# Performance work log

Measured on AMD Instinct MI355X. Metric: run time of the kernel, lower is better.

The kernel has to match this reference:

```python
import jax, jax.numpy as jnp
import numpy as np
from jax import lax

DIM = 96
HEADS = 4
HID = int(DIM * 2.66)  # 255
EPS_LN = 1e-5
EPS_NORM = 1e-12


def _ln(x, w, b):
    # channel-wise LayerNorm over c of (b,c,h,w) (equivalent to to_3d -> LN(c) -> to_4d)
    mu = x.mean(axis=1, keepdims=True)
    var = ((x - mu) ** 2).mean(axis=1, keepdims=True)
    return (x - mu) / jnp.sqrt(var + EPS_LN) * w[None, :, None, None] + b[None, :, None, None]


def _c1x1(w, x):
    # 1x1 conv, no bias: w (out,in), x (b,in,h,w)
    return jnp.einsum('oc,bchw->bohw', w, x)


def _l2norm(x):
    # F.normalize along last dim (pixels), eps=1e-12
    n = jnp.sqrt(jnp.sum(x * x, axis=-1, keepdims=True))
    return x / jnp.maximum(n, EPS_NORM)


def setup_inputs() -> dict:
    key = jax.random.key(0)
    ks = jax.random.split(key, 10)
    B, H, W = 4, 256, 256
    s = 0.02
    return {
        'x': jax.random.normal(ks[0], (B, DIM, H, W), jnp.float32),
        'svp_fea': jax.random.normal(ks[1], (B, 3, H, W), jnp.float32),
        'norm1_w': jnp.ones((DIM,), jnp.float32),
        'norm1_b': jnp.zeros((DIM,), jnp.float32),
        'qkv_w': jax.random.normal(ks[2], (3 * DIM, DIM), jnp.float32) * s,
        'qkv_dw_w': jax.random.normal(ks[3], (3 * DIM, 1, 3, 3), jnp.float32) * s,
        'svp_w': jax.random.normal(ks[4], (3 * HEADS, 3), jnp.float32) * s,
        'temperature': jnp.ones((HEADS, 1, 1), jnp.float32),
        'proj_out_w': jax.random.normal(ks[5], (DIM, DIM + 3 * HEADS), jnp.float32) * s,
        'norm2_w': jnp.ones((DIM,), jnp.float32),
        'norm2_b': jnp.zeros((DIM,), jnp.float32),
        'ffn1_w': jax.random.normal(ks[6], (HID, DIM), jnp.float32) * s,
        'ffn2_w': jax.random.normal(ks[7], (HID, DIM), jnp.float32) * s,
        'ffn_out_w': jax.random.normal(ks[8], (DIM, HID), jnp.float32) * s,
    }


def reference(x, svp_fea, norm1_w, norm1_b, qkv_w, qkv_dw_w, svp_w, temperature,
              proj_out_w, norm2_w, norm2_b, ffn1_w, ffn2_w, ffn_out_w):
    b, c, h, w = x.shape
    hw = h * w
    # --- IlluminationGuideAttention ---
    xn = _ln(x, norm1_w, norm1_b)
    qkv = _c1x1(qkv_w, xn)
    qkv = lax.conv_general_dilated(
        qkv, qkv_dw_w, window_strides=(1, 1), padding='SAME',
        feature_group_count=3 * DIM, dimension_numbers=('NCHW', 'OIHW', 'NCHW'))
    q, k, v = jnp.split(qkv, 3, axis=1)
    svp_q = _c1x1(svp_w, svp_fea)

    def heads(t):
        return t.reshape(b, HEADS, -1, hw)  # b head c (h w)

    q = _l2norm(heads(q))          # (b,H,ch,hw)
    k = _l2norm(heads(k))
    svp_q = _l2norm(heads(svp_q))  # (b,H,3,hw)
    v = heads(v)
    q = jnp.concatenate([q, svp_q], axis=2)  # (b,H,ch+3,hw)

    attn = jnp.einsum('bhcn,bhdn->bhcd', q, k) * temperature[None]
    attn = jax.nn.softmax(attn, axis=-1)
    out = jnp.einsum('bhcd,bhdn->bhcn', attn, v).reshape(b, -1, h, w)
    x = x + _c1x1(proj_out_w, out)

    # --- DualGatedFeedForward ---
    xn = _ln(x, norm2_w, norm2_b)
    p1 = _c1x1(ffn1_w, xn)
    p2 = _c1x1(ffn2_w, xn)
    g = p1 * jax.nn.sigmoid(p2) + p2 * jax.nn.gelu(p1, approximate=False)
    return x + _c1x1(ffn_out_w, g)
```

## Files before the change

kernel.cpp:

```cpp
#include <hip/hip_runtime.h>


namespace {
constexpr int kB = 4;
constexpr int kC = 96;
constexpr int kHW = 65536;
constexpr int kNP = kB * kHW;
constexpr int kQKVC = 288;
constexpr int kNH = 4;
constexpr int kCH = 24;
constexpr int kQC = 27;
constexpr int kHID = 255;
constexpr int kSTR = 40;
constexpr int kQKSPLIT = 32;
}

typedef __attribute__((ext_vector_type(8))) short short8;
typedef __attribute__((ext_vector_type(8))) unsigned short ushort8;
typedef __attribute__((ext_vector_type(4))) float floatx4;

__device__ __forceinline__ float bf2f(unsigned short u) {
  return __uint_as_float(((unsigned int)u) << 16);
}
__device__ __forceinline__ unsigned short f2bf(float f) {
  unsigned int i = __float_as_uint(f);
  i += 0x7fffu + ((i >> 16) & 1u);
  return (unsigned short)(i >> 16);
}

__global__ void k_zero(float* __restrict__ p, int n) {
  const int i = blockIdx.x * blockDim.x + threadIdx.x;
  if (i < n) p[i] = 0.f;
}
__global__ void k_fill0_f32(float* __restrict__ p, int n) {
  const int i = blockIdx.x * blockDim.x + threadIdx.x;
  if (i < n) p[i] = 0.f;
}

__global__ __launch_bounds__(256) void k_wconv(
    const float* __restrict__ qkvw, const float* __restrict__ projw,
    const float* __restrict__ w1, const float* __restrict__ w2,
    const float* __restrict__ fw, unsigned short* __restrict__ qb,
    unsigned short* __restrict__ pb, unsigned short* __restrict__ w1b,
    unsigned short* __restrict__ w2b, unsigned short* __restrict__ fwb) {
  int i = blockIdx.x * 256 + threadIdx.x;
  if (i < 27648) { qb[i] = f2bf(qkvw[i]); return; }
  i -= 27648;
  if (i < 12288) {
    const int r = i >> 7, k = i & 127;
    pb[i] = (k < 108) ? f2bf(projw[r * 108 + k]) : (unsigned short)0;
    return;
  }
  i -= 12288;
  if (i < 24576) { w1b[i] = (i < 24480) ? f2bf(w1[i]) : (unsigned short)0; return; }
  i -= 24576;
  if (i < 24576) { w2b[i] = (i < 24480) ? f2bf(w2[i]) : (unsigned short)0; return; }
  i -= 24576;
  {
    const int r = i >> 8, k = i & 255;
    fwb[i] = (k < 255) ? f2bf(fw[r * 255 + k]) : (unsigned short)0;
  }
}

__global__ __launch_bounds__(256) void k_ln1_apply(
    const float* __restrict__ x, const float* __restrict__ nw,
    const float* __restrict__ nb, unsigned short* __restrict__ A) {
  const int pg = blockIdx.x * 256 + threadIdx.x;
  const int b = pg >> 16, p = pg & (kHW - 1);
  const float* xb = x + (size_t)b * kC * kHW + p;
  float v[kC];
  float s = 0.f, s2 = 0.f;
  #pragma unroll
  for (int c = 0; c < kC; ++c) {
    v[c] = xb[(size_t)c * kHW];
    s += v[c];
    s2 = fmaf(v[c], v[c], s2);
  }
  const float m = s * (1.f / kC);
  const float var = s2 * (1.f / kC) - m * m;
  const float rstd = rsqrtf(var + 1e-5f);
  unsigned short* ob = A + ((size_t)b * kQKVC + 192) * kHW + p;
  #pragma unroll
  for (int c = 0; c < kC; ++c) {
    ob[(size_t)c * kHW] = f2bf((v[c] - m) * rstd * nw[c] + nb[c]);
  }
}

__global__ __launch_bounds__(256) void k_ln2_stats(
    const unsigned short* __restrict__ x2, float* __restrict__ mu, float* __restrict__ rs) {
  const int pg = blockIdx.x * 256 + threadIdx.x;
  const int b = pg >> 16, p = pg & (kHW - 1);
  const unsigned short* xb = x2 + (size_t)b * kC * kHW + p;
  float s = 0.f, s2 = 0.f;
  for (int c = 0; c < kC; ++c) { const float v = bf2f(xb[(size_t)c * kHW]); s += v; s2 += v * v; }
  const float m = s * (1.f / kC);
  const float var = s2 * (1.f / kC) - m * m;
  mu[pg] = m;
  rs[pg] = rsqrtf(var + 1e-5f);
}

__global__ __launch_bounds__(256) void k_gemm_qkv(
    const unsigned short* __restrict__ xn1base, const unsigned short* __restrict__ qb,
    int grp, unsigned short* __restrict__ bufC) {
  __shared__ __align__(16) unsigned short As[96 * kSTR];
  __shared__ __align__(16) unsigned short Bs[128 * kSTR];
  const int tid = threadIdx.x;
  const int b = blockIdx.y;
  const int p0 = blockIdx.x * 128;
  const int wave = tid >> 6, lane = tid & 63, ln16 = lane & 15, quad = lane >> 4;
  floatx4 acc[6][2];
  #pragma unroll
  for (int i = 0; i < 6; ++i) { acc[i][0] = (floatx4)(0.f); acc[i][1] = (floatx4)(0.f); }
  const int rB = tid >> 3, c0 = (tid & 7) * 16;
  const int pos = rB ^ ((tid & 3) << 3);
  const int q0 = (quad ^ ((wave * 2) & 3)) << 3;
  const int q1 = (quad ^ ((wave * 2 + 1) & 3)) << 3;
  for (int ks = 0; ks < 3; ++ks) {
    const int k0 = ks * 32;
    for (int idx = tid; idx < 384; idx += 256) {
      const int m = idx >> 2, ch = idx & 3;
      *(short8*)&As[m * kSTR + ch * 8] =
          *(const short8*)(qb + (size_t)(grp * 96 + m) * 96 + k0 + ch * 8);
    }
    {
      const unsigned short* src =
          xn1base + ((size_t)b * kQKVC + 192 + k0 + rB) * kHW + p0 + c0;
      const ushort8 u0 = ((const ushort8*)src)[0];
      const ushort8 u1 = ((const ushort8*)src)[1];
      #pragma unroll
      for (int e = 0; e < 8; ++e) {
        Bs[(c0 + e) * kSTR + pos] = u0[e];
        Bs[(c0 + 8 + e) * kSTR + pos] = u1[e];
      }
    }
    __syncthreads();
    short8 bfr0 = *(const short8*)&Bs[(wave * 32 + ln16) * kSTR + q0];
    short8 bfr1 = *(const short8*)&Bs[(wave * 32 + 16 + ln16) * kSTR + q1];
    #pragma unroll
    for (int ms = 0; ms < 6; ++ms) {
      const short8 afr = *(const short8*)&As[(ms * 16 + ln16) * kSTR + quad * 8];
      acc[ms][0] = __builtin_amdgcn_mfma_f32_16x16x32_bf16(afr, bfr0, acc[ms][0], 0, 0, 0);
      acc[ms][1] = __builtin_amdgcn_mfma_f32_16x16x32_bf16(afr, bfr1, acc[ms][1], 0, 0, 0);
    }
    __syncthreads();
  }
  unsigned short* ob = bufC + (size_t)b * kC * kHW;
  #pragma unroll
  for (int ms = 0; ms < 6; ++ms)
    #pragma unroll
    for (int ns = 0; ns < 2; ++ns)
      #pragma unroll
      for (int r = 0; r < 4; ++r) {
        const int R = ms * 16 + quad * 4 + r;
        const int P = p0 + wave * 32 + ns * 16 + ln16;
        ob[(size_t)R * kHW + P] = f2bf(acc[ms][ns][r]);
      }
}

__global__ __launch_bounds__(256) void k_gemm_proj(
    const unsigned short* __restrict__ qkv_post, const unsigned short* __restrict__ pb,
    const float* __restrict__ x, unsigned short* __restrict__ x2) {
  __shared__ __align__(16) unsigned short As[96 * kSTR];
  __shared__ __align__(16) unsigned short Bs[128 * kSTR];
  const int tid = threadIdx.x;
  const int b = blockIdx.y;
  const int p0 = blockIdx.x * 128;
  const int wave = tid >> 6, lane = tid & 63, ln16 = lane & 15, quad = lane >> 4;
  floatx4 acc[6][2];
  #pragma unroll
  for (int i = 0; i < 6; ++i) { acc[i][0] = (floatx4)(0.f); acc[i][1] = (floatx4)(0.f); }
  const int rB = tid >> 3, c0 = (tid & 7) * 16;
  const int pos = rB ^ ((tid & 3) << 3);
  const int q0 = (quad ^ ((wave * 2) & 3)) << 3;
  const int q1 = (quad ^ ((wave * 2 + 1) & 3)) << 3;
  for (int ks = 0; ks < 4; ++ks) {
    const int k0 = ks * 32;
    for (int idx = tid; idx < 384; idx += 256) {
      const int m = idx >> 2, ch = idx & 3;
      *(short8*)&As[m * kSTR + ch * 8] =
          *(const short8*)(pb + (size_t)m * 128 + k0 + ch * 8);
    }
    {
      const int k = k0 + rB;
      if (k < 108) {
        const unsigned short* src = qkv_post + ((size_t)b * kQKVC + k) * kHW + p0 + c0;
        const ushort8 u0 = ((const ushort8*)src)[0];
        const ushort8 u1 = ((const ushort8*)src)[1];
        #pragma unroll
        for (int e = 0; e < 8; ++e) {
          Bs[(c0 + e) * kSTR + pos] = u0[e];
          Bs[(c0 + 8 + e) * kSTR + pos] = u1[e];
        }
      } else {
        #pragma unroll
        for (int e = 0; e < 16; ++e) Bs[(c0 + e) * kSTR + pos] = 0;
      }
    }
    __syncthreads();
    short8 bfr0 = *(const short8*)&Bs[(wave * 32 + ln16) * kSTR + q0];
    short8 bfr1 = *(const short8*)&Bs[(wave * 32 + 16 + ln16) * kSTR + q1];
    #pragma unroll
    for (int ms = 0; ms < 6; ++ms) {
      const short8 afr = *(const short8*)&As[(ms * 16 + ln16) * kSTR + quad * 8];
      acc[ms][0] = __builtin_amdgcn_mfma_f32_16x16x32_bf16(afr, bfr0, acc[ms][0], 0, 0, 0);
      acc[ms][1] = __builtin_amdgcn_mfma_f32_16x16x32_bf16(afr, bfr1, acc[ms][1], 0, 0, 0);
    }
    __syncthreads();
  }
  #pragma unroll
  for (int ms = 0; ms < 6; ++ms)
    #pragma unroll
    for (int ns = 0; ns < 2; ++ns)
      #pragma unroll
      for (int r = 0; r < 4; ++r) {
        const int R = ms * 16 + quad * 4 + r;
        const int P = p0 + wave * 32 + ns * 16 + ln16;
        const size_t idx = ((size_t)b * kC + R) * kHW + P;
        x2[idx] = f2bf(acc[ms][ns][r] + x[idx]);
      }
}

__global__ __launch_bounds__(256) void k_gemm_gate(
    const unsigned short* __restrict__ x2, const float* __restrict__ mu_buf,
    const float* __restrict__ rs_buf, const float* __restrict__ nw,
    const float* __restrict__ nb, const unsigned short* __restrict__ w1b,
    const unsigned short* __restrict__ w2b, unsigned short* __restrict__ g) {
  __shared__ __align__(16) unsigned short Bs[3 * 128 * kSTR];
  __shared__ __align__(16) unsigned short As[128 * kSTR];
  __shared__ float mus[128], rss[128];
  const int tid = threadIdx.x;
  const int b = blockIdx.y;
  const int p0 = blockIdx.x * 128;
  if (tid < 128) {
    mus[tid] = mu_buf[(b << 16) + p0 + tid];
    rss[tid] = rs_buf[(b << 16) + p0 + tid];
  }
  __syncthreads();
  const int wave = tid >> 6, lane = tid & 63, ln16 = lane & 15, quad = lane >> 4;
  const int rB = tid >> 3, c0 = (tid & 7) * 16;
  const int pos = rB ^ ((tid & 3) << 3);
  const int q0 = (quad ^ ((wave * 2) & 3)) << 3;
  const int q1 = (quad ^ ((wave * 2 + 1) & 3)) << 3;
  #pragma unroll
  for (int ks = 0; ks < 3; ++ks) {
    const int k = ks * 32 + rB;
    const float wk = nw[k], bk = nb[k];
    const unsigned short* src = x2 + ((size_t)b * kC + k) * kHW + p0 + c0;
    const ushort8 u0 = ((const ushort8*)src)[0];
    const ushort8 u1 = ((const ushort8*)src)[1];
    unsigned short* bp = &Bs[ks * 128 * kSTR];
    #pragma unroll
    for (int e = 0; e < 8; ++e) {
      const int n0 = c0 + e, n1 = c0 + 8 + e;
      bp[n0 * kSTR + pos] = f2bf((bf2f(u0[e]) - mus[n0]) * rss[n0] * wk + bk);
      bp[n1 * kSTR + pos] = f2bf((bf2f(u1[e]) - mus[n1]) * rss[n1] * wk + bk);
    }
  }
  for (int grp = 0; grp < 4; ++grp) {
    const int i0 = grp * 64;
    floatx4 acc[8][2];
    #pragma unroll
    for (int i = 0; i < 8; ++i) { acc[i][0] = (floatx4)(0.f); acc[i][1] = (floatx4)(0.f); }
    #pragma unroll
    for (int ks = 0; ks < 3; ++ks) {
      for (int idx = tid; idx < 512; idx += 256) {
        const int m = idx >> 2, ch = idx & 3;
        const int ii = i0 + (m & 63);
        const unsigned short* wsrc =
            ((m < 64) ? w1b : w2b) + (size_t)ii * 96 + ks * 32 + ch * 8;
        *(short8*)&As[m * kSTR + ch * 8] = *(const short8*)wsrc;
      }
      __syncthreads();
      const unsigned short* bp = &Bs[ks * 128 * kSTR];
      short8 bfr0 = *(const short8*)&bp[(wave * 32 + ln16) * kSTR + q0];
      short8 bfr1 = *(const short8*)&bp[(wave * 32 + 16 + ln16) * kSTR + q1];
      #pragma unroll
      for (int ms = 0; ms < 8; ++ms) {
        const short8 afr = *(const short8*)&As[(ms * 16 + ln16) * kSTR + quad * 8];
        acc[ms][0] = __builtin_amdgcn_mfma_f32_16x16x32_bf16(afr, bfr0, acc[ms][0], 0, 0, 0);
        acc[ms][1] = __builtin_amdgcn_mfma_f32_16x16x32_bf16(afr, bfr1, acc[ms][1], 0, 0, 0);
      }
      __syncthreads();
    }
    #pragma unroll
    for (int ms = 0; ms < 4; ++ms)
      #pragma unroll
      for (int ns = 0; ns < 2; ++ns)
        #pragma unroll
        for (int r = 0; r < 4; ++r) {
          const int ii = i0 + ms * 16 + quad * 4 + r;
          if (ii < kHID) {
            const int P = p0 + wave * 32 + ns * 16 + ln16;
            const float p1 = acc[ms][ns][r], p2 = acc[ms + 4][ns][r];
            const float sig = 1.f / (1.f + __expf(-p2));
            const float gel = 0.5f * p1 * (1.f + erff(p1 * 0.70710678118f));
            g[((size_t)b * kHID + ii) * kHW + P] = f2bf(p1 * sig + p2 * gel);
          }
        }
  }
}

__global__ __launch_bounds__(256) void k_gemm_fout(
    const unsigned short* __restrict__ g, const unsigned short* __restrict__ fwb,
    const unsigned short* __restrict__ x2, float* __restrict__ out) {
  __shared__ __align__(16) unsigned short As[96 * kSTR];
  __shared__ __align__(16) unsigned short Bs[128 * kSTR];
  const int tid = threadIdx.x;
  const int b = blockIdx.y;
  const int p0 = blockIdx.x * 128;
  const int wave = tid >> 6, lane = tid & 63, ln16 = lane & 15, quad = lane >> 4;
  floatx4 acc[6][2];
  #pragma unroll
  for (int i = 0; i < 6; ++i) { acc[i][0] = (floatx4)(0.f); acc[i][1] = (floatx4)(0.f); }
  const int rB = tid >> 3, c0 = (tid & 7) * 16;
  const int pos = rB ^ ((tid & 3) << 3);
  const int q0 = (quad ^ ((wave * 2) & 3)) << 3;
  const int q1 = (quad ^ ((wave * 2 + 1) & 3)) << 3;
  for (int ks = 0; ks < 8; ++ks) {
    const int k0 = ks * 32;
    for (int idx = tid; idx < 384; idx += 256) {
      const int m = idx >> 2, ch = idx & 3;
      *(short8*)&As[m * kSTR + ch * 8] =
          *(const short8*)(fwb + (size_t)m * 256 + k0 + ch * 8);
    }
    {
      const int k = k0 + rB;
      if (k < kHID) {
        const unsigned short* src = g + ((size_t)b * kHID + k) * kHW + p0 + c0;
        const ushort8 u0 = ((const ushort8*)src)[0];
        const ushort8 u1 = ((const ushort8*)src)[1];
        #pragma unroll
        for (int e = 0; e < 8; ++e) {
          Bs[(c0 + e) * kSTR + pos] = u0[e];
          Bs[(c0 + 8 + e) * kSTR + pos] = u1[e];
        }
      } else {
        #pragma unroll
        for (int e = 0; e < 16; ++e) Bs[(c0 + e) * kSTR + pos] = 0;
      }
    }
    __syncthreads();
    short8 bfr0 = *(const short8*)&Bs[(wave * 32 + ln16) * kSTR + q0];
    short8 bfr1 = *(const short8*)&Bs[(wave * 32 + 16 + ln16) * kSTR + q1];
    #pragma unroll
    for (int ms = 0; ms < 6; ++ms) {
      const short8 afr = *(const short8*)&As[(ms * 16 + ln16) * kSTR + quad * 8];
      acc[ms][0] = __builtin_amdgcn_mfma_f32_16x16x32_bf16(afr, bfr0, acc[ms][0], 0, 0, 0);
      acc[ms][1] = __builtin_amdgcn_mfma_f32_16x16x32_bf16(afr, bfr1, acc[ms][1], 0, 0, 0);
    }
    __syncthreads();
  }
  #pragma unroll
  for (int ms = 0; ms < 6; ++ms)
    #pragma unroll
    for (int ns = 0; ns < 2; ++ns)
      #pragma unroll
      for (int r = 0; r < 4; ++r) {
        const int R = ms * 16 + quad * 4 + r;
        const int P = p0 + wave * 32 + ns * 16 + ln16;
        const size_t idx = ((size_t)b * kC + R) * kHW + P;
        out[idx] = acc[ms][ns][r] + bf2f(x2[idx]);
      }
}

__global__ __launch_bounds__(256) void k_dw(
    const unsigned short* __restrict__ buf, const float* __restrict__ dww,
    unsigned short* __restrict__ qkv_post, int gbase) {
  const int blk = blockIdx.x;
  const int plane = blk >> 5;
  const int y0 = (blk & 31) * 8;
  const int b = plane / kC, chl = plane % kC;
  const int t = threadIdx.x;
  const int y = y0 + (t >> 5);
  const int x0 = (t & 31) * 8;
  const unsigned short* in = buf + (size_t)plane * kHW;
  float w[9];
  #pragma unroll
  for (int i = 0; i < 9; ++i) w[i] = dww[(size_t)(gbase + chl) * 9 + i];
  float acc[8];
  #pragma unroll
  for (int j = 0; j < 8; ++j) acc[j] = 0.f;
  #pragma unroll
  for (int dy = -1; dy <= 1; ++dy) {
    const int yy = y + dy;
    if (yy < 0 || yy > 255) continue;
    const unsigned short* rp = in + yy * 256;
    float f[10];
    const ushort8 v = *(const ushort8*)(rp + x0);
    #pragma unroll
    for (int e = 0; e < 8; ++e) f[e + 1] = bf2f(v[e]);
    f[0] = (x0 > 0) ? bf2f(rp[x0 - 1]) : 0.f;
    f[9] = (x0 < 248) ? bf2f(rp[x0 + 8]) : 0.f;
    const float w0 = w[(dy + 1) * 3], w1 = w[(dy + 1) * 3 + 1], w2 = w[(dy + 1) * 3 + 2];
    #pragma unroll
    for (int j = 0; j < 8; ++j)
      acc[j] = fmaf(w0, f[j], fmaf(w1, f[j + 1], fmaf(w2, f[j + 2], acc[j])));
  }
  unsigned short* op = qkv_post + ((size_t)b * kQKVC + gbase + chl) * kHW + y * 256 + x0;
  ushort8 o;
  #pragma unroll
  for (int j = 0; j < 8; ++j) o[j] = f2bf(acc[j]);
  *(ushort8*)op = o;
}

__global__ __launch_bounds__(256) void k_svpq(
    const float* __restrict__ svp, const float* __restrict__ svpw,
    unsigned short* __restrict__ svpq) {
  const int pg = blockIdx.x * 256 + threadIdx.x;
  const int b = pg >> 16, p = pg & (kHW - 1);
  const float s0 = svp[((size_t)b * 3 + 0) * kHW + p];
  const float s1 = svp[((size_t)b * 3 + 1) * kHW + p];
  const float s2 = svp[((size_t)b * 3 + 2) * kHW + p];
  #pragma unroll
  for (int j = 0; j < 12; ++j) {
    const float v = svpw[j * 3] * s0 + svpw[j * 3 + 1] * s1 + svpw[j * 3 + 2] * s2;
    svpq[((size_t)b * 12 + j) * kHW + p] = f2bf(v);
  }
}

__global__ __launch_bounds__(256) void k_qk(
    const unsigned short* __restrict__ qkv_post, const unsigned short* __restrict__ svpq,
    float* __restrict__ spart, float* __restrict__ ssbuf) {
  const int bh = blockIdx.y, b = bh >> 2, h = bh & 3;
  const int tid = threadIdx.x;
  const int wave = tid >> 6, lane = tid & 63;
  const int l15 = lane & 15, gq = lane >> 4;
  const int pstart = blockIdx.x * 2048 + wave * 512;
  constexpr int NCH = 16;

  const unsigned short* pA0 =
      qkv_post + ((size_t)b * kQKVC + h * kCH + l15) * kHW + gq * 8;
  const unsigned short* pB0 =
      qkv_post + ((size_t)b * kQKVC + 96 + h * kCH + l15) * kHW + gq * 8;
  const int rA1 = 16 + l15, rB1 = 16 + l15;
  const bool vA1 = (rA1 < kQC), vB1 = (rB1 < kCH);
  const unsigned short* pA1 =
      (rA1 < kCH) ? qkv_post + ((size_t)b * kQKVC + h * kCH + rA1) * kHW + gq * 8
      : (rA1 < kQC) ? svpq + ((size_t)(b * 12 + h * 3 + (rA1 - kCH))) * kHW + gq * 8
                    : pA0;
  const unsigned short* pB1 =
      vB1 ? qkv_post + ((size_t)b * kQKVC + 96 + h * kCH + rB1) * kHW + gq * 8 : pB0;

  floatx4 c00 = (floatx4)(0.f), c01 = (floatx4)(0.f);
  floatx4 c10 = (floatx4)(0.f), c11 = (floatx4)(0.f);
  float ssA0 = 0.f, ssA1 = 0.f, ssB0 = 0.f, ssB1 = 0.f;
  const short8 kZ = (short8)(short)0;

  short8 a0 = *(const short8*)(pA0 + pstart);
  short8 b0 = *(const short8*)(pB0 + pstart);
  short8 a1 = vA1 ? *(const short8*)(pA1 + pstart) : kZ;
  short8 b1 = vB1 ? *(const short8*)(pB1 + pstart) : kZ;
  for (int c = 0; c < NCH; ++c) {
    const short8 ta0 = a0, tb0 = b0, ta1 = a1, tb1 = b1;
    if (c + 1 < NCH) {
      const int pn = pstart + (c + 1) * 32;
      a0 = *(const short8*)(pA0 + pn);
      b0 = *(const short8*)(pB0 + pn);
      a1 = vA1 ? *(const short8*)(pA1 + pn) : kZ;
      b1 = vB1 ? *(const short8*)(pB1 + pn) : kZ;
    }
    c00 = __builtin_amdgcn_mfma_f32_16x16x32_bf16(ta0, tb0, c00, 0, 0, 0);
    c01 = __builtin_amdgcn_mfma_f32_16x16x32_bf16(ta0, tb1, c01, 0, 0, 0);
    c10 = __builtin_amdgcn_mfma_f32_16x16x32_bf16(ta1, tb0, c10, 0, 0, 0);
    c11 = __builtin_amdgcn_mfma_f32_16x16x32_bf16(ta1, tb1, c11, 0, 0, 0);
    #pragma unroll
    for (int e = 0; e < 8; ++e) {
      const float v0 = bf2f((unsigned short)ta0[e]);
      const float v1 = bf2f((unsigned short)ta1[e]);
      const float v2 = bf2f((unsigned short)tb0[e]);
      const float v3 = bf2f((unsigned short)tb1[e]);
      ssA0 = fmaf(v0, v0, ssA0);
      ssA1 = fmaf(v1, v1, ssA1);
      ssB0 = fmaf(v2, v2, ssB0);
      ssB1 = fmaf(v3, v3, ssB1);
    }
  }
  ssA0 += __shfl_xor(ssA0, 16); ssA0 += __shfl_xor(ssA0, 32);
  ssA1 += __shfl_xor(ssA1, 16); ssA1 += __shfl_xor(ssA1, 32);
  ssB0 += __shfl_xor(ssB0, 16); ssB0 += __shfl_xor(ssB0, 32);
  ssB1 += __shfl_xor(ssB1, 16); ssB1 += __shfl_xor(ssB1, 32);
  if (gq == 0) {
    atomicAdd(&ssbuf[b * 96 + h * kCH + l15], ssA0);
    if (rA1 < kCH) atomicAdd(&ssbuf[b * 96 + h * kCH + rA1], ssA1);
    else if (rA1 < kQC) atomicAdd(&ssbuf[768 + b * 12 + h * 3 + (rA1 - kCH)], ssA1);
    atomicAdd(&ssbuf[384 + b * 96 + h * kCH + l15], ssB0);
    if (vB1) atomicAdd(&ssbuf[384 + b * 96 + h * kCH + rB1], ssB1);
  }
  float* wp = spart + ((size_t)((blockIdx.x * 16 + bh) * 4 + wave)) * 648;
  #pragma unroll
  for (int r = 0; r < 4; ++r) {
    const int row0 = gq * 4 + r, row1 = 16 + gq * 4 + r;
    wp[row0 * kCH + l15] = c00[r];
    if (16 + l15 < kCH) wp[row0 * kCH + 16 + l15] = c01[r];
    if (row1 < kQC) {
      wp[row1 * kCH + l15] = c10[r];
      if (16 + l15 < kCH) wp[row1 * kCH + 16 + l15] = c11[r];
    }
  }
}

__global__ __launch_bounds__(256) void k_softmax(
    const float* __restrict__ spart, const float* __restrict__ ssbuf,
    const float* __restrict__ temp, float* __restrict__ attn) {
  const int row = blockIdx.x * 256 + threadIdx.x;
  if (row >= kB * kNH * kQC) return;
  const int bh = row / kQC, c = row - bh * kQC;
  const int b = bh >> 2, h = bh & 3;
  const float ssq = (c < kCH) ? ssbuf[b * 96 + h * kCH + c]
                              : ssbuf[768 + b * 12 + h * 3 + (c - kCH)];
  const float rq = 1.f / fmaxf(sqrtf(ssq), 1e-12f);
  const float t = temp[h];
  float l[kCH];
  #pragma unroll
  for (int d = 0; d < kCH; ++d) l[d] = 0.f;
  for (int s = 0; s < kQKSPLIT * 4; ++s) {
    const int split = s >> 2, wv = s & 3;
    const float* sp = spart + ((size_t)((split * 16 + bh) * 4 + wv)) * 648 + c * kCH;
    #pragma unroll
    for (int d = 0; d < kCH; ++d) l[d] += sp[d];
  }
  float mx = -1e30f;
  #pragma unroll
  for (int d = 0; d < kCH; ++d) {
    const float rk = 1.f / fmaxf(sqrtf(ssbuf[384 + b * 96 + h * kCH + d]), 1e-12f);
    l[d] = l[d] * rq * rk * t;
    mx = fmaxf(mx, l[d]);
  }
  float sum = 0.f;
  #pragma unroll
  for (int d = 0; d < kCH; ++d) { l[d] = __expf(l[d] - mx); sum += l[d]; }
  const float inv = 1.f / sum;
  float* arow = attn + (size_t)(bh * kQC + c) * kCH;
  #pragma unroll
  for (int d = 0; d < kCH; ++d) arow[d] = l[d] * inv;
}

__global__ __launch_bounds__(256) void k_av(
    const float* __restrict__ attn, unsigned short* __restrict__ qkv_post) {
  const int h = blockIdx.y;
  const int pg = blockIdx.x * 256 + threadIdx.x;
  const int b = pg >> 16, p = pg & (kHW - 1);
  __shared__ float at[kQC * kCH];
  for (int idx = threadIdx.x; idx < kQC * kCH; idx += 256)
    at[idx] = attn[(size_t)(b * kNH + h) * kQC * kCH + idx];
  __syncthreads();
  float acc[kQC];
  #pragma unroll
  for (int c = 0; c < kQC; ++c) acc[c] = 0.f;
  for (int d = 0; d < kCH; ++d) {
    const float vv = bf2f(qkv_post[((size_t)b * kQKVC + 192 + h * kCH + d) * kHW + p]);
    #pragma unroll
    for (int c = 0; c < kQC; ++c) acc[c] += at[c * kCH + d] * vv;
  }
  #pragma unroll
  for (int c = 0; c < kQC; ++c)
    qkv_post[((size_t)b * kQKVC + h * kQC + c) * kHW + p] = f2bf(acc[c]);
}

extern "C" void kernel_launch(void* const* d_in, const int* in_sizes, int n_in,
                              void* d_out, int out_size, void* d_ws, size_t ws_size,
                              hipStream_t stream) {
  (void)in_sizes; (void)n_in;
  const float* x     = (const float*)d_in[0];
  const float* svp   = (const float*)d_in[1];
  const float* n1w   = (const float*)d_in[2];
  const float* n1b   = (const float*)d_in[3];
  const float* qkvw  = (const float*)d_in[4];
  const float* dww   = (const float*)d_in[5];
  const float* svpw  = (const float*)d_in[6];
  const float* temp  = (const float*)d_in[7];
  const float* projw = (const float*)d_in[8];
  const float* n2w   = (const float*)d_in[9];
  const float* n2b   = (const float*)d_in[10];
  const float* w1    = (const float*)d_in[11];
  const float* w2    = (const float*)d_in[12];
  const float* fw    = (const float*)d_in[13];
  float* outp = (float*)d_out;

  const size_t SZ_A = (size_t)kB * kQKVC * kHW * 2;
  const size_t SZ_C = (size_t)kB * kC * kHW * 2;
  const size_t NEED = (1u << 20) + SZ_A + SZ_C;

  if (ws_size < NEED) {
    k_fill0_f32<<<(out_size + 255) / 256, 256, 0, stream>>>(outp, out_size);
    return;
  }

  char* ws = (char*)d_ws;
  float* attn  = (float*)(ws + 65536);
  float* ssbuf = (float*)(ws + 131072);
  unsigned short* qb  = (unsigned short*)(ws + 262144);
  unsigned short* pb  = (unsigned short*)(ws + 317440);
  unsigned short* w1b = (unsigned short*)(ws + 342016);
  unsigned short* w2b = (unsigned short*)(ws + 391168);
  unsigned short* fwb = (unsigned short*)(ws + 440320);
  unsigned short* A    = (unsigned short*)(ws + (1u << 20));
  unsigned short* bufC = (unsigned short*)(ws + (1u << 20) + SZ_A);
  float* mu2 = (float*)(ws + (1u << 20) + 134u * 1048576u);
  float* rs2 = (float*)(ws + (1u << 20) + 135u * 1048576u);
  unsigned short* g    = A;
  unsigned short* x2   = bufC;
  unsigned short* svpq = bufC;
  float* spart = (float*)(ws + (1u << 20) + SZ_A + 8u * 1048576u);

  k_wconv<<<444, 256, 0, stream>>>(qkvw, projw, w1, w2, fw, qb, pb, w1b, w2b, fwb);
  k_zero<<<4, 256, 0, stream>>>(ssbuf, 816);
  k_ln1_apply<<<kNP / 256, 256, 0, stream>>>(x, n1w, n1b, A);
  for (int grp = 0; grp < 3; ++grp) {
    k_gemm_qkv<<<dim3(kHW / 128, kB), 256, 0, stream>>>(A, qb, grp, bufC);
    k_dw<<<kB * kC * 32, 256, 0, stream>>>(bufC, dww, A, grp * kC);
  }
  k_svpq<<<kNP / 256, 256, 0, stream>>>(svp, svpw, svpq);
  k_qk<<<dim3(kQKSPLIT, 16), 256, 0, stream>>>(A, svpq, spart, ssbuf);
  k_softmax<<<2, 256, 0, stream>>>(spart, ssbuf, temp, attn);
  k_av<<<dim3(kNP / 256, kNH), 256, 0, stream>>>(attn, A);
  k_gemm_proj<<<dim3(kHW / 128, kB), 256, 0, stream>>>(A, pb, x, x2);
  k_ln2_stats<<<kNP / 256, 256, 0, stream>>>(x2, mu2, rs2);
  k_gemm_gate<<<dim3(kHW / 128, kB), 256, 0, stream>>>(x2, mu2, rs2, n2w, n2b, w1b, w2b, g);
  k_gemm_fout<<<dim3(kHW / 128, kB), 256, 0, stream>>>(g, fwb, x2, outp);
}
```

Before: 757.2 us.

## Vectorize per-pixel kernels and use tanh-approx GELU with fast reciprocal

```diff
diff --git a/kernel.cpp b/kernel.cpp
--- a/kernel.cpp
+++ b/kernel.cpp
@@ -17,6 +17,7 @@
 
 typedef __attribute__((ext_vector_type(8))) short short8;
 typedef __attribute__((ext_vector_type(8))) unsigned short ushort8;
+typedef __attribute__((ext_vector_type(4))) unsigned short ushortx4;
 typedef __attribute__((ext_vector_type(4))) float floatx4;
 
 __device__ __forceinline__ float bf2f(unsigned short u) {
@@ -88,15 +89,29 @@
 
 __global__ __launch_bounds__(256) void k_ln2_stats(
     const unsigned short* __restrict__ x2, float* __restrict__ mu, float* __restrict__ rs) {
-  const int pg = blockIdx.x * 256 + threadIdx.x;
-  const int b = pg >> 16, p = pg & (kHW - 1);
-  const unsigned short* xb = x2 + (size_t)b * kC * kHW + p;
-  float s = 0.f, s2 = 0.f;
-  for (int c = 0; c < kC; ++c) { const float v = bf2f(xb[(size_t)c * kHW]); s += v; s2 += v * v; }
-  const float m = s * (1.f / kC);
-  const float var = s2 * (1.f / kC) - m * m;
-  mu[pg] = m;
-  rs[pg] = rsqrtf(var + 1e-5f);
+  const int t8 = blockIdx.x * 256 + threadIdx.x;
+  const int b = t8 >> 13, p0 = (t8 & 8191) * 8;
+  const unsigned short* xb = x2 + (size_t)b * kC * kHW + p0;
+  float s[8], s2[8];
+  #pragma unroll
+  for (int j = 0; j < 8; ++j) { s[j] = 0.f; s2[j] = 0.f; }
+  for (int c = 0; c < kC; ++c) {
+    const ushort8 u = *(const ushort8*)&xb[(size_t)c * kHW];
+    #pragma unroll
+    for (int j = 0; j < 8; ++j) {
+      const float v = bf2f(u[j]);
+      s[j] += v;
+      s2[j] = fmaf(v, v, s2[j]);
+    }
+  }
+  const int base = (b << 16) + p0;
+  #pragma unroll
+  for (int j = 0; j < 8; ++j) {
+    const float m = s[j] * (1.f / kC);
+    const float var = s2[j] * (1.f / kC) - m * m;
+    mu[base + j] = m;
+    rs[base + j] = rsqrtf(var + 1e-5f);
+  }
 }
 
 __global__ __launch_bounds__(256) void k_gemm_qkv(
@@ -292,9 +307,10 @@
           if (ii < kHID) {
             const int P = p0 + wave * 32 + ns * 16 + ln16;
             const float p1 = acc[ms][ns][r], p2 = acc[ms + 4][ns][r];
-            const float sig = 1.f / (1.f + __expf(-p2));
-            const float gel = 0.5f * p1 * (1.f + erff(p1 * 0.70710678118f));
-            g[((size_t)b * kHID + ii) * kHW + P] = f2bf(p1 * sig + p2 * gel);
+            const float sig = __builtin_amdgcn_rcpf(1.f + __expf(-p2));
+            const float targ = p1 * fmaf(p1 * p1, 0.0713548f, 1.5957691f);
+            const float gel = p1 * __builtin_amdgcn_rcpf(1.f + __expf(-targ));
+            g[((size_t)b * kHID + ii) * kHW + P] = f2bf(fmaf(p1, sig, p2 * gel));
           }
         }
   }
@@ -406,15 +422,23 @@
 __global__ __launch_bounds__(256) void k_svpq(
     const float* __restrict__ svp, const float* __restrict__ svpw,
     unsigned short* __restrict__ svpq) {
-  const int pg = blockIdx.x * 256 + threadIdx.x;
-  const int b = pg >> 16, p = pg & (kHW - 1);
-  const float s0 = svp[((size_t)b * 3 + 0) * kHW + p];
-  const float s1 = svp[((size_t)b * 3 + 1) * kHW + p];
-  const float s2 = svp[((size_t)b * 3 + 2) * kHW + p];
-  #pragma unroll
-  for (int j = 0; j < 12; ++j) {
-    const float v = svpw[j * 3] * s0 + svpw[j * 3 + 1] * s1 + svpw[j * 3 + 2] * s2;
-    svpq[((size_t)b * 12 + j) * kHW + p] = f2bf(v);
+  const int t8 = blockIdx.x * 256 + threadIdx.x;
+  const int b = t8 >> 13, p0 = (t8 & 8191) * 8;
+  float s0[8], s1[8], s2v[8];
+  #pragma unroll
+  for (int j = 0; j < 8; ++j) {
+    s0[j] = svp[((size_t)b * 3 + 0) * kHW + p0 + j];
+    s1[j] = svp[((size_t)b * 3 + 1) * kHW + p0 + j];
+    s2v[j] = svp[((size_t)b * 3 + 2) * kHW + p0 + j];
+  }
+  #pragma unroll
+  for (int jj = 0; jj < 12; ++jj) {
+    const float w0 = svpw[jj * 3], w1 = svpw[jj * 3 + 1], w2 = svpw[jj * 3 + 2];
+    ushort8 o;
+    #pragma unroll
+    for (int j = 0; j < 8; ++j)
+      o[j] = f2bf(fmaf(w2, s2v[j], fmaf(w1, s1[j], w0 * s0[j])));
+    *(ushort8*)&svpq[((size_t)b * 12 + jj) * kHW + p0] = o;
   }
 }
 
@@ -538,23 +562,37 @@
 __global__ __launch_bounds__(256) void k_av(
     const float* __restrict__ attn, unsigned short* __restrict__ qkv_post) {
   const int h = blockIdx.y;
-  const int pg = blockIdx.x * 256 + threadIdx.x;
-  const int b = pg >> 16, p = pg & (kHW - 1);
+  const int t4 = blockIdx.x * 256 + threadIdx.x;
+  const int b = t4 >> 14, p0 = (t4 & 16383) * 4;
   __shared__ float at[kQC * kCH];
   for (int idx = threadIdx.x; idx < kQC * kCH; idx += 256)
     at[idx] = attn[(size_t)(b * kNH + h) * kQC * kCH + idx];
   __syncthreads();
-  float acc[kQC];
-  #pragma unroll
-  for (int c = 0; c < kQC; ++c) acc[c] = 0.f;
+  float acc[kQC][4];
+  #pragma unroll
+  for (int c = 0; c < kQC; ++c)
+    #pragma unroll
+    for (int j = 0; j < 4; ++j) acc[c][j] = 0.f;
   for (int d = 0; d < kCH; ++d) {
-    const float vv = bf2f(qkv_post[((size_t)b * kQKVC + 192 + h * kCH + d) * kHW + p]);
-    #pragma unroll
-    for (int c = 0; c < kQC; ++c) acc[c] += at[c * kCH + d] * vv;
-  }
-  #pragma unroll
-  for (int c = 0; c < kQC; ++c)
-    qkv_post[((size_t)b * kQKVC + h * kQC + c) * kHW + p] = f2bf(acc[c]);
+    const ushortx4 v =
+        *(const ushortx4*)&qkv_post[((size_t)b * kQKVC + 192 + h * kCH + d) * kHW + p0];
+    float vv[4];
+    #pragma unroll
+    for (int j = 0; j < 4; ++j) vv[j] = bf2f(v[j]);
+    #pragma unroll
+    for (int c = 0; c < kQC; ++c) {
+      const float a = at[c * kCH + d];
+      #pragma unroll
+      for (int j = 0; j < 4; ++j) acc[c][j] = fmaf(a, vv[j], acc[c][j]);
+    }
+  }
+  #pragma unroll
+  for (int c = 0; c < kQC; ++c) {
+    ushortx4 o;
+    #pragma unroll
+    for (int j = 0; j < 4; ++j) o[j] = f2bf(acc[c][j]);
+    *(ushortx4*)&qkv_post[((size_t)b * kQKVC + h * kQC + c) * kHW + p0] = o;
+  }
 }
 
 extern "C" void kernel_launch(void* const* d_in, const int* in_sizes, int n_in,
@@ -610,12 +648,12 @@
     k_gemm_qkv<<<dim3(kHW / 128, kB), 256, 0, stream>>>(A, qb, grp, bufC);
     k_dw<<<kB * kC * 32, 256, 0, stream>>>(bufC, dww, A, grp * kC);
   }
-  k_svpq<<<kNP / 256, 256, 0, stream>>>(svp, svpw, svpq);
+  k_svpq<<<kNP / 8 / 256, 256, 0, stream>>>(svp, svpw, svpq);
   k_qk<<<dim3(kQKSPLIT, 16), 256, 0, stream>>>(A, svpq, spart, ssbuf);
   k_softmax<<<2, 256, 0, stream>>>(spart, ssbuf, temp, attn);
-  k_av<<<dim3(kNP / 256, kNH), 256, 0, stream>>>(attn, A);
+  k_av<<<dim3(kNP / 4 / 256, kNH), 256, 0, stream>>>(attn, A);
   k_gemm_proj<<<dim3(kHW / 128, kB), 256, 0, stream>>>(A, pb, x, x2);
-  k_ln2_stats<<<kNP / 256, 256, 0, stream>>>(x2, mu2, rs2);
+  k_ln2_stats<<<kNP / 8 / 256, 256, 0, stream>>>(x2, mu2, rs2);
   k_gemm_gate<<<dim3(kHW / 128, kB), 256, 0, stream>>>(x2, mu2, rs2, n2w, n2b, w1b, w2b, g);
   k_gemm_fout<<<dim3(kHW / 128, kB), 256, 0, stream>>>(g, fwb, x2, outp);
 }
```

New measurement: 716.3 us. -5.4%, faster.
